# Performance work log

Measured on AMD Instinct MI355X. Metric: run time of the kernel, lower is better.

The kernel has to match this reference:

```python
import jax, jax.numpy as jnp
import numpy as np

N_HEADS = 8
EMBED = 640
CROSS = 768
HEAD = EMBED // N_HEADS


def setup_inputs() -> dict:
    key = jax.random.key(0)
    ks = jax.random.split(key, 10)
    s_e = 1.0 / np.sqrt(EMBED)
    s_c = 1.0 / np.sqrt(CROSS)
    return {
        "x": jax.random.normal(ks[0], (8, 4096, EMBED), jnp.float32),
        "y": jax.random.normal(ks[1], (8, 77, CROSS), jnp.float32),
        "Wq": jax.random.uniform(ks[2], (EMBED, EMBED), jnp.float32, -s_e, s_e),
        "bq": jax.random.uniform(ks[3], (EMBED,), jnp.float32, -s_e, s_e),
        "Wk": jax.random.uniform(ks[4], (CROSS, EMBED), jnp.float32, -s_c, s_c),
        "bk": jax.random.uniform(ks[5], (EMBED,), jnp.float32, -s_c, s_c),
        "Wv": jax.random.uniform(ks[6], (CROSS, EMBED), jnp.float32, -s_c, s_c),
        "bv": jax.random.uniform(ks[7], (EMBED,), jnp.float32, -s_c, s_c),
        "Wo": jax.random.uniform(ks[8], (EMBED, EMBED), jnp.float32, -s_e, s_e),
        "bo": jax.random.uniform(ks[9], (EMBED,), jnp.float32, -s_e, s_e),
    }


def reference(x, y, Wq, bq, Wk, bk, Wv, bv, Wo, bo):
    B, T, C = x.shape
    S = y.shape[1]
    # projections; split heads: [B, H, T, D]
    q = (x @ Wq + bq).reshape(B, T, N_HEADS, HEAD).transpose(0, 2, 1, 3)
    k = (y @ Wk + bk).reshape(B, S, N_HEADS, HEAD).transpose(0, 2, 1, 3)
    v = (y @ Wv + bv).reshape(B, S, N_HEADS, HEAD).transpose(0, 2, 1, 3)
    scores = jnp.einsum("bhtd,bhsd->bhts", q, k) / jnp.sqrt(jnp.float32(HEAD))
    attn = jax.nn.softmax(scores, axis=-1)
    out = jnp.einsum("bhts,bhsd->bhtd", attn, v)
    out = out.transpose(0, 2, 1, 3).reshape(B, T, C)
    return out @ Wo + bo
```

## Files before the change

### kernel.cpp

```cpp
#include <hip/hip_runtime.h>
#include <hip/hip_bf16.h>
#include <hip/hip_fp16.h>

#define EMBED 640
#define CROSS 768
#define NH 8
#define HEAD 80
#define BATCH 8
#define SEQT 4096
#define SEQS 77
#define MROWS (BATCH * SEQT)

typedef _Float16 half8 __attribute__((ext_vector_type(8)));
typedef float floatx4 __attribute__((ext_vector_type(4)));

__device__ __forceinline__ void lds_load16(const void* g, void* l) {
    __builtin_amdgcn_global_load_lds(
        (const __attribute__((address_space(1))) void*)g,
        (__attribute__((address_space(3))) void*)l, 16, 0, 0);
}

__global__ __launch_bounds__(256) void cvt_f32_f16(
    const float* __restrict__ in, _Float16* __restrict__ out)
{
    size_t i = ((size_t)blockIdx.x * 256 + threadIdx.x) * 8;
    float4 a = *(const float4*)&in[i];
    float4 b = *(const float4*)&in[i + 4];
    half8 h;
    h[0] = (_Float16)a.x; h[1] = (_Float16)a.y;
    h[2] = (_Float16)a.z; h[3] = (_Float16)a.w;
    h[4] = (_Float16)b.x; h[5] = (_Float16)b.y;
    h[6] = (_Float16)b.z; h[7] = (_Float16)b.w;
    *(half8*)&out[i] = h;
}

__global__ __launch_bounds__(256) void transpose_all(
    const float* __restrict__ Wq, const float* __restrict__ Wo,
    const float* __restrict__ Wk, const float* __restrict__ Wv,
    _Float16* __restrict__ wqt, _Float16* __restrict__ wot,
    _Float16* __restrict__ wkt, _Float16* __restrict__ wvt)
{
    __shared__ float t[32][33];
    const int z = blockIdx.z;
    const float* W;  _Float16* Wt;  int K;
    if      (z == 0) { W = Wq; Wt = wqt; K = EMBED; }
    else if (z == 1) { W = Wo; Wt = wot; K = EMBED; }
    else if (z == 2) { W = Wk; Wt = wkt; K = CROSS; }
    else             { W = Wv; Wt = wvt; K = CROSS; }
    const int N = EMBED;
    const int k0 = blockIdx.y * 32, n0 = blockIdx.x * 32;
    if (k0 >= K) return;
    for (int r = threadIdx.y; r < 32; r += 8)
        t[r][threadIdx.x] = W[(size_t)(k0 + r) * N + n0 + threadIdx.x];
    __syncthreads();
    for (int r = threadIdx.y; r < 32; r += 8)
        Wt[(size_t)(n0 + r) * K + k0 + threadIdx.x] = (_Float16)t[threadIdx.x][r];
}

__global__ __launch_bounds__(256) void cvt_y_zero(
    const float* __restrict__ y, _Float16* __restrict__ yh,
    _Float16* __restrict__ vth)
{
    const size_t i = (size_t)blockIdx.x * 256 + threadIdx.x;
    if (i < (size_t)640 * CROSS / 8) {
        const size_t e = i * 8;
        half8 h = {};
        if (e < (size_t)BATCH * SEQS * CROSS) {
            float4 a = *(const float4*)&y[e];
            float4 b = *(const float4*)&y[e + 4];
            h[0] = (_Float16)a.x; h[1] = (_Float16)a.y;
            h[2] = (_Float16)a.z; h[3] = (_Float16)a.w;
            h[4] = (_Float16)b.x; h[5] = (_Float16)b.y;
            h[6] = (_Float16)b.z; h[7] = (_Float16)b.w;
        }
        *(half8*)&yh[e] = h;
    } else {
        const size_t j = (i - (size_t)640 * CROSS / 8) * 8;
        *(half8*)&vth[j] = (half8){};
    }
}

template <bool HALF_OUT>
__global__ __launch_bounds__(256) void gemm_f16(
    const _Float16* __restrict__ A,
    const _Float16* __restrict__ Bt,
    const float* __restrict__ bias,
    void* __restrict__ Cout, int M, int N, int K, float scale)
{
    __shared__ _Float16 As[3][128 * 32];
    __shared__ _Float16 Bs[3][128 * 32];

    const int tid  = threadIdx.x;
    const int wave = tid >> 6;
    const int lane = tid & 63;
    const int quad = lane >> 4;
    const int l16  = lane & 15;

    const int l   = blockIdx.y * gridDim.x + blockIdx.x;
    const int inner = l >> 3;
    const int p   = (l & 7) + 8 * (inner / gridDim.x);
    const int nt  = inner % gridDim.x;
    const int m0 = p * 128, n0 = nt * 128;
    const int wm = (wave >> 1) * 64, wn = (wave & 1) * 64;

    const int row = tid >> 2;
    const int kch = ((tid & 3) ^ ((row >> 1) & 3)) * 8;
    const int cq  = (quad ^ ((l16 >> 1) & 3)) * 8;

    const _Float16* pa0 = &A [(size_t)(m0 + row)      * K + kch];
    const _Float16* pa1 = &A [(size_t)(m0 + 64 + row) * K + kch];
    const _Float16* pb0 = &Bt[(size_t)(n0 + row)      * K + kch];
    const _Float16* pb1 = &Bt[(size_t)(n0 + 64 + row) * K + kch];

    const int NT = K / 32;

    auto stage = [&](int t) {
        const int bf = t % 3;
        const int off = t * 32;
        lds_load16(pa0 + off, &As[bf][wave * 512]);
        lds_load16(pa1 + off, &As[bf][2048 + wave * 512]);
        lds_load16(pb0 + off, &Bs[bf][wave * 512]);
        lds_load16(pb1 + off, &Bs[bf][2048 + wave * 512]);
    };
    stage(0); stage(1);

    floatx4 acc[4][4] = {};

    for (int t = 0; t < NT; ++t) {
        if (t < NT - 1) asm volatile("s_waitcnt vmcnt(4)" ::: "memory");
        else            asm volatile("s_waitcnt vmcnt(0)" ::: "memory");
        __builtin_amdgcn_s_barrier();
        if (t + 2 < NT) stage(t + 2);

        const _Float16* as = As[t % 3];
        const _Float16* bs = Bs[t % 3];
        half8 a[4], b[4];
        #pragma unroll
        for (int i = 0; i < 4; ++i)
            a[i] = *(const half8*)&as[(wm + i * 16 + l16) * 32 + cq];
        #pragma unroll
        for (int j = 0; j < 4; ++j)
            b[j] = *(const half8*)&bs[(wn + j * 16 + l16) * 32 + cq];
        #pragma unroll
        for (int i = 0; i < 4; ++i)
            #pragma unroll
            for (int j = 0; j < 4; ++j)
                acc[i][j] = __builtin_amdgcn_mfma_f32_16x16x32_f16(
                    a[i], b[j], acc[i][j], 0, 0, 0);
    }

    float bcol[4];
    #pragma unroll
    for (int j = 0; j < 4; ++j) bcol[j] = bias[n0 + wn + j * 16 + l16];
    #pragma unroll
    for (int i = 0; i < 4; ++i)
        #pragma unroll
        for (int r = 0; r < 4; ++r) {
            const int m = m0 + wm + i * 16 + quad * 4 + r;
            #pragma unroll
            for (int j = 0; j < 4; ++j) {
                float v = (acc[i][j][r] + bcol[j]) * scale;
                const size_t off = (size_t)m * N + n0 + wn + j * 16 + l16;
                if (HALF_OUT) ((_Float16*)Cout)[off] = (_Float16)v;
                else          ((float*)Cout)[off] = v;
            }
        }
}

__global__ __launch_bounds__(256) void kv_gemm(
    const _Float16* __restrict__ yh,
    const _Float16* __restrict__ Wkt, const _Float16* __restrict__ Wvt,
    const float* __restrict__ bk, const float* __restrict__ bv,
    _Float16* __restrict__ kh, _Float16* __restrict__ vth)
{
    __shared__ _Float16 As[64 * 32];
    __shared__ _Float16 Bs[64 * 32];

    const int tid = threadIdx.x;
    const int wave = tid >> 6, lane = tid & 63;
    const int quad = lane >> 4, l16 = lane & 15;
    const int m0 = blockIdx.y * 64, n0 = blockIdx.x * 64;
    const bool isV = blockIdx.z != 0;
    const _Float16* Bt = isV ? Wvt : Wkt;
    const float* bias  = isV ? bv : bk;

    const int row = tid >> 2;
    const int kch = (tid & 3) * 8;

    floatx4 acc[4] = {};

    for (int k0 = 0; k0 < CROSS; k0 += 32) {
        lds_load16(&yh[(size_t)(m0 + row) * CROSS + k0 + kch], &As[wave * 512]);
        lds_load16(&Bt[(size_t)(n0 + row) * CROSS + k0 + kch], &Bs[wave * 512]);
        __syncthreads();
        half8 b = *(const half8*)&Bs[(wave * 16 + l16) * 32 + quad * 8];
        #pragma unroll
        for (int i = 0; i < 4; ++i) {
            half8 a = *(const half8*)&As[(i * 16 + l16) * 32 + quad * 8];
            acc[i] = __builtin_amdgcn_mfma_f32_16x16x32_f16(a, b, acc[i], 0, 0, 0);
        }
        __syncthreads();
    }

    const int n = n0 + wave * 16 + l16;
    const int h = n / HEAD, d = n % HEAD;
    const float bb = bias[n];
    #pragma unroll
    for (int i = 0; i < 4; ++i)
        #pragma unroll
        for (int r = 0; r < 4; ++r) {
            const int m = m0 + i * 16 + quad * 4 + r;
            if (m >= BATCH * SEQS) continue;
            const int b_ = m / SEQS, s = m % SEQS;
            const int bh = b_ * NH + h;
            const float v = acc[i][r] + bb;
            if (isV) vth[(size_t)bh * (HEAD * 80) + d * 80 + s] = (_Float16)v;
            else     kh [(size_t)bh * (SEQS * HEAD) + s * HEAD + d] = (_Float16)v;
        }
}

__global__ __launch_bounds__(256, 4) void attn_mfma(
    const _Float16* __restrict__ qh,
    const _Float16* __restrict__ kh,
    const _Float16* __restrict__ vth,
    _Float16* __restrict__ oh)
{
    constexpr int LS = 88;
    __shared__ _Float16 lds[(80 + 80 + 64) * LS + 8];
    _Float16* Ks = lds;
    _Float16* Vt = lds + 80 * LS;
    _Float16* Ps = lds + 160 * LS;

    const int tid = threadIdx.x;
    const int wave = tid >> 6, lane = tid & 63;
    const int quad = lane >> 4, l16 = lane & 15;
    const int bh = blockIdx.y;
    const int b = bh >> 3, h = bh & 7;
    const size_t row0 = (size_t)b * SEQT + (size_t)blockIdx.x * 256;
    const half8 hz = {};

    const _Float16* qp = qh + (row0 + wave * 16 + l16) * EMBED + h * HEAD;

    half8 qa0 = *(const half8*)&qp[quad * 8];
    half8 qa1 = *(const half8*)&qp[32 + quad * 8];
    half8 qa2 = (quad < 2) ? *(const half8*)&qp[64 + quad * 8] : hz;

    for (int idx = tid; idx < 80 * 11; idx += 256) {
        const int s = idx / 11, c = idx % 11;
        half8 v = hz;
        if (s < SEQS && c < 10)
            v = *(const half8*)&kh[(size_t)bh * (SEQS * HEAD) + s * HEAD + c * 8];
        *(half8*)&Ks[s * LS + c * 8] = v;
    }
    for (int idx = tid; idx < 80 * 11; idx += 256) {
        const int d = idx / 11, c = idx % 11;
        half8 v = hz;
        if (c < 10)
            v = *(const half8*)&vth[(size_t)bh * (HEAD * 80) + d * 80 + c * 8];
        *(half8*)&Vt[d * LS + c * 8] = v;
    }
    __syncthreads();

    for (int t = 0; t < 4; ++t) {
        floatx4 accs[5] = {};
        #pragma unroll
        for (int st = 0; st < 5; ++st) {
            const _Float16* kr = &Ks[(st * 16 + l16) * LS];
            half8 b0 = *(const half8*)&kr[quad * 8];
            half8 b1 = *(const half8*)&kr[32 + quad * 8];
            half8 b2 = *(const half8*)&kr[64 + quad * 8];
            accs[st] = __builtin_amdgcn_mfma_f32_16x16x32_f16(qa0, b0, accs[st], 0, 0, 0);
            accs[st] = __builtin_amdgcn_mfma_f32_16x16x32_f16(qa1, b1, accs[st], 0, 0, 0);
            accs[st] = __builtin_amdgcn_mfma_f32_16x16x32_f16(qa2, b2, accs[st], 0, 0, 0);
        }
        if (l16 >= 13) {
            accs[4][0] = -1e30f; accs[4][1] = -1e30f;
            accs[4][2] = -1e30f; accs[4][3] = -1e30f;
        }

        float recip[4];
        #pragma unroll
        for (int r = 0; r < 4; ++r) {
            float m = accs[0][r];
            #pragma unroll
            for (int st = 1; st < 5; ++st) m = fmaxf(m, accs[st][r]);
            m = fmaxf(m, __shfl_xor(m, 1));
            m = fmaxf(m, __shfl_xor(m, 2));
            m = fmaxf(m, __shfl_xor(m, 4));
            m = fmaxf(m, __shfl_xor(m, 8));
            float l = 0.f;
            const int row = wave * 16 + quad * 4 + r;
            #pragma unroll
            for (int st = 0; st < 5; ++st) {
                float e = __expf(accs[st][r] - m);
                l += e;
                Ps[row * LS + st * 16 + l16] = (_Float16)e;
            }
            l += __shfl_xor(l, 1);
            l += __shfl_xor(l, 2);
            l += __shfl_xor(l, 4);
            l += __shfl_xor(l, 8);
            recip[r] = 1.0f / l;
        }
        __syncthreads();

        half8 qn0 = hz, qn1 = hz, qn2 = hz;
        if (t < 3) {
            const _Float16* qn = qp + (size_t)(t + 1) * 64 * EMBED;
            qn0 = *(const half8*)&qn[quad * 8];
            qn1 = *(const half8*)&qn[32 + quad * 8];
            if (quad < 2) qn2 = *(const half8*)&qn[64 + quad * 8];
        }

        const _Float16* pr = &Ps[(wave * 16 + l16) * LS];
        half8 pa0 = *(const half8*)&pr[quad * 8];
        half8 pa1 = *(const half8*)&pr[32 + quad * 8];
        half8 pa2 = (quad < 2) ? *(const half8*)&pr[64 + quad * 8] : hz;
        __syncthreads();

        floatx4 acco[5] = {};
        #pragma unroll
        for (int dt = 0; dt < 5; ++dt) {
            const _Float16* vr = &Vt[(dt * 16 + l16) * LS];
            half8 b0 = *(const half8*)&vr[quad * 8];
            half8 b1 = *(const half8*)&vr[32 + quad * 8];
            half8 b2 = *(const half8*)&vr[64 + quad * 8];
            acco[dt] = __builtin_amdgcn_mfma_f32_16x16x32_f16(pa0, b0, acco[dt], 0, 0, 0);
            acco[dt] = __builtin_amdgcn_mfma_f32_16x16x32_f16(pa1, b1, acco[dt], 0, 0, 0);
            acco[dt] = __builtin_amdgcn_mfma_f32_16x16x32_f16(pa2, b2, acco[dt], 0, 0, 0);
        }

        #pragma unroll
        for (int r = 0; r < 4; ++r) {
            const size_t grow = row0 + t * 64 + wave * 16 + quad * 4 + r;
            #pragma unroll
            for (int dt = 0; dt < 5; ++dt)
                oh[grow * EMBED + h * HEAD + dt * 16 + l16] =
                    (_Float16)(acco[dt][r] * recip[r]);
        }

        qa0 = qn0; qa1 = qn1; qa2 = qn2;
    }
}

extern "C" void kernel_launch(void* const* d_in, const int* in_sizes, int n_in,
                              void* d_out, int out_size, void* d_ws, size_t ws_size,
                              hipStream_t stream)
{
    const float* x  = (const float*)d_in[0];
    const float* y  = (const float*)d_in[1];
    const float* Wq = (const float*)d_in[2];
    const float* bq = (const float*)d_in[3];
    const float* Wk = (const float*)d_in[4];
    const float* bk = (const float*)d_in[5];
    const float* Wv = (const float*)d_in[6];
    const float* bv = (const float*)d_in[7];
    const float* Wo = (const float*)d_in[8];
    const float* bo = (const float*)d_in[9];
    float* out = (float*)d_out;

    const size_t ME = (size_t)MROWS * EMBED;
    _Float16* xh  = (_Float16*)d_ws;
    _Float16* qh  = xh + ME;
    _Float16* ah  = qh + ME;
    _Float16* kh  = ah + ME;
    _Float16* vth = kh  + (size_t)BATCH * NH * SEQS * HEAD;
    _Float16* wqt = vth + (size_t)BATCH * NH * HEAD * 80;
    _Float16* wot = wqt + (size_t)EMBED * EMBED;
    _Float16* yh  = wot + (size_t)EMBED * EMBED;
    _Float16* wkt = yh  + (size_t)640 * CROSS;
    _Float16* wvt = wkt + (size_t)EMBED * CROSS;

    transpose_all<<<dim3(EMBED / 32, CROSS / 32, 4), dim3(32, 8), 0, stream>>>(
        Wq, Wo, Wk, Wv, wqt, wot, wkt, wvt);
    cvt_y_zero<<<dim3(440), 256, 0, stream>>>(y, yh, vth);
    cvt_f32_f16<<<dim3(ME / (256 * 8)), 256, 0, stream>>>(x, xh);

    gemm_f16<true><<<dim3(EMBED / 128, MROWS / 128), 256, 0, stream>>>(
        xh, wqt, bq, qh, MROWS, EMBED, EMBED, 0.11180339887498949f);
    kv_gemm<<<dim3(EMBED / 64, 640 / 64, 2), 256, 0, stream>>>(
        yh, wkt, wvt, bk, bv, kh, vth);
    attn_mfma<<<dim3(SEQT / 256, BATCH * NH), 256, 0, stream>>>(qh, kh, vth, ah);
    gemm_f16<false><<<dim3(EMBED / 128, MROWS / 128), 256, 0, stream>>>(
        ah, wot, bo, out, MROWS, EMBED, EMBED, 1.0f);
}
```

Measured before the change: 294.3 us.

## Restructure GEMM pipeline to double-buffered BK=64 tiles with new swizzle

Changes the f16 GEMM mainloop from a triple-buffered K=32 pipeline to a double-buffered K=64 pipeline. This halves the number of barrier iterations and adds a new XOR swizzle over 8 chunks. It also adds setprio around the MFMA block and an extra barrier per iteration. LDS usage grows from 48KB to 64KB, which may reduce occupancy, and prefetch depth drops from two stages to one.

```diff
diff --git a/kernel.cpp b/kernel.cpp
--- a/kernel.cpp
+++ b/kernel.cpp
@@ -87,8 +87,8 @@
     const float* __restrict__ bias,
     void* __restrict__ Cout, int M, int N, int K, float scale)
 {
-    __shared__ _Float16 As[3][128 * 32];
-    __shared__ _Float16 Bs[3][128 * 32];
+    __shared__ _Float16 As[2][128 * 64];
+    __shared__ _Float16 Bs[2][128 * 64];
 
     const int tid  = threadIdx.x;
     const int wave = tid >> 6;
@@ -103,50 +103,67 @@
     const int m0 = p * 128, n0 = nt * 128;
     const int wm = (wave >> 1) * 64, wn = (wave & 1) * 64;
 
-    const int row = tid >> 2;
-    const int kch = ((tid & 3) ^ ((row >> 1) & 3)) * 8;
-    const int cq  = (quad ^ ((l16 >> 1) & 3)) * 8;
-
-    const _Float16* pa0 = &A [(size_t)(m0 + row)      * K + kch];
-    const _Float16* pa1 = &A [(size_t)(m0 + 64 + row) * K + kch];
-    const _Float16* pb0 = &Bt[(size_t)(n0 + row)      * K + kch];
-    const _Float16* pb1 = &Bt[(size_t)(n0 + 64 + row) * K + kch];
-
-    const int NT = K / 32;
-
-    auto stage = [&](int t) {
-        const int bf = t % 3;
-        const int off = t * 32;
-        lds_load16(pa0 + off, &As[bf][wave * 512]);
-        lds_load16(pa1 + off, &As[bf][2048 + wave * 512]);
-        lds_load16(pb0 + off, &Bs[bf][wave * 512]);
-        lds_load16(pb1 + off, &Bs[bf][2048 + wave * 512]);
+    const int srow = wave * 32 + (lane >> 3);
+    const int sch  = ((lane & 7) ^ (lane >> 3)) * 8;
+    const _Float16* gA[4];
+    const _Float16* gB[4];
+    #pragma unroll
+    for (int q = 0; q < 4; ++q) {
+        gA[q] = &A [(size_t)(m0 + srow + q * 8) * K + sch];
+        gB[q] = &Bt[(size_t)(n0 + srow + q * 8) * K + sch];
+    }
+
+    const int NT = K / 64;
+
+    auto stage = [&](int t, int bf) {
+        const size_t off = (size_t)t * 64;
+        #pragma unroll
+        for (int q = 0; q < 4; ++q) {
+            lds_load16(gA[q] + off, &As[bf][(wave * 4 + q) * 512]);
+            lds_load16(gB[q] + off, &Bs[bf][(wave * 4 + q) * 512]);
+        }
     };
-    stage(0); stage(1);
+    stage(0, 0);
 
     floatx4 acc[4][4] = {};
 
     for (int t = 0; t < NT; ++t) {
-        if (t < NT - 1) asm volatile("s_waitcnt vmcnt(4)" ::: "memory");
-        else            asm volatile("s_waitcnt vmcnt(0)" ::: "memory");
+        const int bf = t & 1;
+        if (t + 1 < NT) {
+            stage(t + 1, bf ^ 1);
+            asm volatile("s_waitcnt vmcnt(8)" ::: "memory");
+        } else {
+            asm volatile("s_waitcnt vmcnt(0)" ::: "memory");
+        }
         __builtin_amdgcn_s_barrier();
-        if (t + 2 < NT) stage(t + 2);
-
-        const _Float16* as = As[t % 3];
-        const _Float16* bs = Bs[t % 3];
-        half8 a[4], b[4];
-        #pragma unroll
-        for (int i = 0; i < 4; ++i)
-            a[i] = *(const half8*)&as[(wm + i * 16 + l16) * 32 + cq];
-        #pragma unroll
-        for (int j = 0; j < 4; ++j)
-            b[j] = *(const half8*)&bs[(wn + j * 16 + l16) * 32 + cq];
-        #pragma unroll
-        for (int i = 0; i < 4; ++i)
+        __builtin_amdgcn_sched_barrier(0);
+
+        const _Float16* as = As[bf];
+        const _Float16* bs = Bs[bf];
+        __builtin_amdgcn_s_setprio(1);
+        #pragma unroll
+        for (int k = 0; k < 2; ++k) {
+            half8 a[4], b[4];
+            #pragma unroll
+            for (int i = 0; i < 4; ++i)
+                a[i] = *(const half8*)&as[(wm + i * 16 + l16) * 64 +
+                                          (((k * 4 + quad) ^ (l16 & 7)) * 8)];
             #pragma unroll
             for (int j = 0; j < 4; ++j)
-                acc[i][j] = __builtin_amdgcn_mfma_f32_16x16x32_f16(
-                    a[i], b[j], acc[i][j], 0, 0, 0);
+                b[j] = *(const half8*)&bs[(wn + j * 16 + l16) * 64 +
+                                          (((k * 4 + quad) ^ (l16 & 7)) * 8)];
+            #pragma unroll
+            for (int i = 0; i < 4; ++i)
+                #pragma unroll
+                for (int j = 0; j < 4; ++j)
+                    acc[i][j] = __builtin_amdgcn_mfma_f32_16x16x32_f16(
+                        a[i], b[j], acc[i][j], 0, 0, 0);
+        }
+        __builtin_amdgcn_s_setprio(0);
+
+        asm volatile("s_waitcnt lgkmcnt(0)" ::: "memory");
+        __builtin_amdgcn_sched_barrier(0);
+        __builtin_amdgcn_s_barrier();
     }
 
     float bcol[4];
```

After: 288.2 us. -2.1%, faster.
